# Kernel optimization log

Hardware: AMD Instinct MI355X
Metric: run time of the kernel (lower is better)

## Reference

```python
import jax, jax.numpy as jnp
import numpy as np

B, S, D, H = 2, 2048, 1024, 16
HD = D // H  # 64


def setup_inputs() -> dict:
    key = jax.random.key(0)
    ks = jax.random.split(key, 9)
    sd = 1.0 / np.sqrt(D)  # torch Linear default init scale (uniform, but normal ok for ref)
    return {
        "x": jax.random.normal(ks[0], (B, S, D), dtype=jnp.float32),
        # torch Linear weight is [out, in]; stack per head -> [H, HD, D]
        "Wq": jax.random.normal(ks[1], (H, HD, D), dtype=jnp.float32) * sd,
        "bq": jax.random.normal(ks[2], (H, HD), dtype=jnp.float32) * sd,
        "Wk": jax.random.normal(ks[3], (H, HD, D), dtype=jnp.float32) * sd,
        "bk": jax.random.normal(ks[4], (H, HD), dtype=jnp.float32) * sd,
        "Wv": jax.random.normal(ks[5], (H, HD, D), dtype=jnp.float32) * sd,
        "bv": jax.random.normal(ks[6], (H, HD), dtype=jnp.float32) * sd,
        "Wp": jax.random.normal(ks[7], (D, D), dtype=jnp.float32) * sd,
        "bp": jax.random.normal(ks[8], (D,), dtype=jnp.float32) * sd,
    }


def reference(x, Wq, bq, Wk, bk, Wv, bv, Wp, bp):
    # Per-head QKV projections, batched over heads: [B,S,D] x [H,HD,D] -> [B,H,S,HD]
    q = jnp.einsum("bsd,hed->bhse", x, Wq) + bq[None, :, None, :]
    k = jnp.einsum("bsd,hed->bhse", x, Wk) + bk[None, :, None, :]
    v = jnp.einsum("bsd,hed->bhse", x, Wv) + bv[None, :, None, :]
    scale = 1.0 / np.sqrt(HD)
    scores = jnp.einsum("bhse,bhte->bhst", q, k) * scale  # [B,H,S,S]
    attn = jax.nn.softmax(scores, axis=-1)
    out = jnp.einsum("bhst,bhte->bhse", attn, v)  # [B,H,S,HD]
    # concat heads along last dim (head-major order matches torch.cat over heads)
    out = out.transpose(0, 2, 1, 3).reshape(x.shape[0], x.shape[1], -1)  # [B,S,D]
    return out @ Wp.T + bp
```

## Files before the change

### kernel.cpp

```cpp
#include <hip/hip_runtime.h>
#include <hip/hip_bf16.h>
#include <stdint.h>

#define B_  2
#define S_  2048
#define D_  1024
#define H_  16
#define HD_ 64
#define M_  (B_*S_)
#define BH_ (B_*H_)

typedef __bf16 bf16;
typedef bf16  bf16x8 __attribute__((ext_vector_type(8)));
typedef bf16  bf16x4 __attribute__((ext_vector_type(4)));
typedef bf16  bf16x2 __attribute__((ext_vector_type(2)));
typedef float f32x4  __attribute__((ext_vector_type(4)));

#define SCALE_LOG2E 0.18033688011112042f
#define MFIX_LOG2E  23.083120654223415f

__device__ __forceinline__ f32x4 mfma16(bf16x8 a, bf16x8 b, f32x4 c) {
    return __builtin_amdgcn_mfma_f32_16x16x32_bf16(a, b, c, 0, 0, 0);
}
__device__ __forceinline__ float fexp2(float x) {
    return __builtin_amdgcn_exp2f(x);
}

__device__ __forceinline__ void gload_lds16(const bf16* g, bf16* l) {
    auto* gp = reinterpret_cast<__attribute__((address_space(1))) uint32_t*>(
        reinterpret_cast<uintptr_t>(const_cast<bf16*>(g)));
    auto* lp = reinterpret_cast<__attribute__((address_space(3))) uint32_t*>(
        reinterpret_cast<uintptr_t>(l));
    __builtin_amdgcn_global_load_lds(gp, lp, 16, 0, 0);
}

__global__ __launch_bounds__(256) void k_convert(
        const float* __restrict__ x,
        const float* __restrict__ wq, const float* __restrict__ wk,
        const float* __restrict__ wv, const float* __restrict__ wp,
        bf16* __restrict__ xb,
        bf16* __restrict__ wqb, bf16* __restrict__ wkb,
        bf16* __restrict__ wvb, bf16* __restrict__ wpb) {
    const int y = blockIdx.y;
    const float* src = (y == 0) ? x : (y == 1) ? wq : (y == 2) ? wk
                     : (y == 3) ? wv : wp;
    bf16* dst        = (y == 0) ? xb : (y == 1) ? wqb : (y == 2) ? wkb
                     : (y == 3) ? wvb : wpb;
    const int reps = (y == 0) ? 4 : 1;
    const int idx = blockIdx.x * 256 + threadIdx.x;
    for (int rep = 0; rep < reps; ++rep) {
        const size_t e = (size_t)rep * (1u << 20) + (size_t)idx * 4;
        const float4 f = *(const float4*)(src + e);
        bf16x4 o;
        o[0] = (bf16)f.x; o[1] = (bf16)f.y; o[2] = (bf16)f.z; o[3] = (bf16)f.w;
        *(bf16x4*)(dst + e) = o;
    }
}

__global__ __launch_bounds__(256) void k_gemm_qkv(
        const bf16* __restrict__ x,
        const bf16* __restrict__ Wq, const bf16* __restrict__ Wk, const bf16* __restrict__ Wv,
        const float* __restrict__ bq, const float* __restrict__ bk, const float* __restrict__ bv,
        bf16* __restrict__ q, bf16* __restrict__ k, bf16* __restrict__ vt) {
    const int z = blockIdx.z;
    const bf16* A   = x;
    const bf16* Bt  = (z == 0) ? Wq : (z == 1) ? Wk : Wv;
    const float* bias = (z == 0) ? bq : (z == 1) ? bk : bv;
    bf16* C         = (z == 0) ? q  : (z == 1) ? k  : vt;

    __shared__ bf16 As[2][128*32];
    __shared__ bf16 Bs[2][128*32];
    const int K = D_;
    const int NIT = K / 32;
    const int tid = threadIdx.x;
    const int w  = tid >> 6, L = tid & 63;
    const int lr = L & 15,  lq = L >> 4;
    const int tileM = blockIdx.y * 128, tileN = blockIdx.x * 128;
    const int wm = (w >> 1) * 64, wn = (w & 1) * 64;

    const f32x4 fzero = {0.f, 0.f, 0.f, 0.f};
    f32x4 acc[4][4];
#pragma unroll
    for (int i = 0; i < 4; ++i)
#pragma unroll
        for (int j = 0; j < 4; ++j) acc[i][j] = fzero;

    const int srow   = L >> 2;
    const int schunk = (L & 3) ^ (srow & 3);
    const bf16* ag = A  + (size_t)(tileM + w*32 + srow) * K + schunk*8;
    const bf16* bg = Bt + (size_t)(tileN + w*32 + srow) * K + schunk*8;
    const int sbase = (w*32)*32;
    const int sw = lr & 3;

    gload_lds16(ag,          &As[0][sbase]);
    gload_lds16(ag + 16*K,   &As[0][sbase + 16*32]);
    gload_lds16(bg,          &Bs[0][sbase]);
    gload_lds16(bg + 16*K,   &Bs[0][sbase + 16*32]);
    __syncthreads();

    for (int it = 0; it < NIT; ++it) {
        const int cur = it & 1, nxt = cur ^ 1;
        if (it + 1 < NIT) {
            const int kt = (it + 1) * 32;
            gload_lds16(ag + kt,          &As[nxt][sbase]);
            gload_lds16(ag + kt + 16*K,   &As[nxt][sbase + 16*32]);
            gload_lds16(bg + kt,          &Bs[nxt][sbase]);
            gload_lds16(bg + kt + 16*K,   &Bs[nxt][sbase + 16*32]);
        }

        bf16x8 af[4], bfr[4];
#pragma unroll
        for (int i = 0; i < 4; ++i)
            af[i]  = *(const bf16x8*)&As[cur][(wm + i*16 + lr)*32 + ((lq ^ sw) * 8)];
#pragma unroll
        for (int j = 0; j < 4; ++j)
            bfr[j] = *(const bf16x8*)&Bs[cur][(wn + j*16 + lr)*32 + ((lq ^ sw) * 8)];
#pragma unroll
        for (int i = 0; i < 4; ++i)
#pragma unroll
            for (int j = 0; j < 4; ++j)
                acc[i][j] = mfma16(af[i], bfr[j], acc[i][j]);

        if (it + 1 < NIT) __syncthreads();
    }

#pragma unroll
    for (int i = 0; i < 4; ++i) {
#pragma unroll
        for (int j = 0; j < 4; ++j) {
            const int m0 = tileM + wm + i*16 + lq*4;
            const int n  = tileN + wn + j*16 + lr;
            const int h = n >> 6, e = n & 63;
            if (z != 2) {
#pragma unroll
                for (int r = 0; r < 4; ++r) {
                    const int m = m0 + r;
                    const int b = m >> 11, s = m & (S_ - 1);
                    C[((size_t)((b*H_ + h)*S_ + s) << 6) + e] =
                        (bf16)(acc[i][j][r] + bias[n]);
                }
            } else {
                const int b = m0 >> 11, s0 = m0 & (S_ - 1);
                const float bn = bias[n];
                bf16x4 t4;
#pragma unroll
                for (int r = 0; r < 4; ++r) t4[r] = (bf16)(acc[i][j][r] + bn);
                *(bf16x4*)&C[(((size_t)(b*H_ + h)*HD_ + e) << 11) + s0] = t4;
            }
        }
    }
}

__global__ __launch_bounds__(256, 4) void k_gemm_proj(
        const bf16* __restrict__ A, const bf16* __restrict__ Bt,
        const float* __restrict__ bias, float* __restrict__ C) {
    __shared__ bf16 As[2][64*32];
    __shared__ bf16 Bs[2][64*32];
    const int K = D_;
    const int NIT = K / 32;
    const int tid = threadIdx.x;
    const int w  = tid >> 6, L = tid & 63;
    const int lr = L & 15,  lq = L >> 4;
    const int tileM = blockIdx.y * 64, tileN = blockIdx.x * 64;
    const int wm = (w >> 1) * 32, wn = (w & 1) * 32;

    const f32x4 fzero = {0.f, 0.f, 0.f, 0.f};
    f32x4 acc[2][2];
#pragma unroll
    for (int i = 0; i < 2; ++i)
#pragma unroll
        for (int j = 0; j < 2; ++j) acc[i][j] = fzero;

    const int srow   = L >> 2;
    const int schunk = (L & 3) ^ (srow & 3);
    const bf16* ag = A  + (size_t)(tileM + w*16 + srow) * K + schunk*8;
    const bf16* bg = Bt + (size_t)(tileN + w*16 + srow) * K + schunk*8;
    const int sbase = (w*16)*32;
    const int sw = lr & 3;

    gload_lds16(ag, &As[0][sbase]);
    gload_lds16(bg, &Bs[0][sbase]);
    __syncthreads();

    for (int it = 0; it < NIT; ++it) {
        const int cur = it & 1, nxt = cur ^ 1;
        if (it + 1 < NIT) {
            const int kt = (it + 1) * 32;
            gload_lds16(ag + kt, &As[nxt][sbase]);
            gload_lds16(bg + kt, &Bs[nxt][sbase]);
        }

        bf16x8 af[2], bfr[2];
#pragma unroll
        for (int i = 0; i < 2; ++i)
            af[i]  = *(const bf16x8*)&As[cur][(wm + i*16 + lr)*32 + ((lq ^ sw) * 8)];
#pragma unroll
        for (int j = 0; j < 2; ++j)
            bfr[j] = *(const bf16x8*)&Bs[cur][(wn + j*16 + lr)*32 + ((lq ^ sw) * 8)];
#pragma unroll
        for (int i = 0; i < 2; ++i)
#pragma unroll
            for (int j = 0; j < 2; ++j)
                acc[i][j] = mfma16(af[i], bfr[j], acc[i][j]);

        if (it + 1 < NIT) __syncthreads();
    }

#pragma unroll
    for (int i = 0; i < 2; ++i) {
#pragma unroll
        for (int j = 0; j < 2; ++j) {
#pragma unroll
            for (int r = 0; r < 4; ++r) {
                const int m = tileM + wm + i*16 + lq*4 + r;
                const int n = tileN + wn + j*16 + lr;
                C[(size_t)m * D_ + n] = acc[i][j][r] + bias[n];
            }
        }
    }
}

__global__ __launch_bounds__(256, 2) void k_attn(const bf16* __restrict__ Q,
                                                 const bf16* __restrict__ Kg,
                                                 const bf16* __restrict__ Vt,
                                                 bf16* __restrict__ O) {
    __shared__ bf16 Ks[2][64*64];
    __shared__ bf16 Vs[2][64*64];
    __shared__ bf16 Ps[4*32*64];
    const int tid = threadIdx.x;
    const int w  = tid >> 6, L = tid & 63;
    const int lr = L & 15,  lq = L >> 4;
    const int bh = blockIdx.y;
    const int q0 = blockIdx.x * 128 + w * 32;
    const size_t base = (size_t)bh * S_ * HD_;
    const bf16* qp = Q  + base;
    const bf16* kp = Kg + base;
    const bf16* vp = Vt + base;

    bf16x8 qf[2][2];
#pragma unroll
    for (int h2 = 0; h2 < 2; ++h2) {
        qf[h2][0] = *(const bf16x8*)&qp[(q0 + h2*16 + lr)*HD_ + lq*8];
        qf[h2][1] = *(const bf16x8*)&qp[(q0 + h2*16 + lr)*HD_ + 32 + lq*8];
    }

    const int rbase = (w & 1) * 32;
    const int srow  = L >> 3;
    const int gchunk = (L & 7) ^ srow;

    const int c0 = ((lq ^ (lr & 7))) * 8;
    const int c1 = ((lq ^ (lr & 7)) ^ 4) * 8;
    const int pxor = lr & 7;

    const f32x4 fzero = {0.f, 0.f, 0.f, 0.f};
    float l_lane[2] = {0.f, 0.f};
    f32x4 o_acc[2][4];
#pragma unroll
    for (int h2 = 0; h2 < 2; ++h2)
#pragma unroll
        for (int eb = 0; eb < 4; ++eb) o_acc[h2][eb] = fzero;

    bf16* myP = &Ps[w * 32 * 64];

    if (w < 2) {
#pragma unroll
        for (int i = 0; i < 4; ++i)
            gload_lds16(kp + (size_t)(rbase + i*8 + srow)*HD_ + gchunk*8,
                        &Ks[0][(rbase + i*8)*HD_]);
    } else {
#pragma unroll
        for (int i = 0; i < 4; ++i)
            gload_lds16(vp + (size_t)(rbase + i*8 + srow)*S_ + gchunk*8,
                        &Vs[0][(rbase + i*8)*HD_]);
    }
    __syncthreads();

    for (int it = 0; it < S_/64; ++it) {
        const int cur = it & 1, nxt = cur ^ 1;
        if (it + 1 < S_/64) {
            const int t1 = (it + 1) * 64;
            if (w < 2) {
#pragma unroll
                for (int i = 0; i < 4; ++i)
                    gload_lds16(kp + (size_t)(t1 + rbase + i*8 + srow)*HD_ + gchunk*8,
                                &Ks[nxt][(rbase + i*8)*HD_]);
            } else {
#pragma unroll
                for (int i = 0; i < 4; ++i)
                    gload_lds16(vp + (size_t)(rbase + i*8 + srow)*S_ + t1 + gchunk*8,
                                &Vs[nxt][(rbase + i*8)*HD_]);
            }
        }

#pragma unroll
        for (int j = 0; j < 4; ++j) {
            const bf16x8 kf0 = *(const bf16x8*)&Ks[cur][(j*16 + lr)*HD_ + c0];
            const bf16x8 kf1 = *(const bf16x8*)&Ks[cur][(j*16 + lr)*HD_ + c1];
            const int key0 = j*16 + lq*4;
            const int poff = ((key0 >> 3) ^ pxor)*8 + (key0 & 7);
#pragma unroll
            for (int h2 = 0; h2 < 2; ++h2) {
                f32x4 z = fzero;
                z = mfma16(kf0, qf[h2][0], z);
                z = mfma16(kf1, qf[h2][1], z);
                bf16x4 t4;
                float ls = 0.f;
#pragma unroll
                for (int r = 0; r < 4; ++r) {
                    const float pv = fexp2(
                        __builtin_fmaf(z[r], SCALE_LOG2E, -MFIX_LOG2E));
                    ls += pv;
                    t4[r] = (bf16)pv;
                }
                l_lane[h2] += ls;
                *(bf16x4*)&myP[(h2*16 + lr)*64 + poff] = t4;
            }
        }

        bf16x8 pb[2][2];
#pragma unroll
        for (int h2 = 0; h2 < 2; ++h2) {
            pb[h2][0] = *(const bf16x8*)&myP[(h2*16 + lr)*64 + ((lq     ^ pxor))*8];
            pb[h2][1] = *(const bf16x8*)&myP[(h2*16 + lr)*64 + (((4+lq) ^ pxor))*8];
        }
#pragma unroll
        for (int eb = 0; eb < 4; ++eb) {
            const bf16x8 vb0 = *(const bf16x8*)&Vs[cur][(eb*16 + lr)*HD_ + c0];
            const bf16x8 vb1 = *(const bf16x8*)&Vs[cur][(eb*16 + lr)*HD_ + c1];
#pragma unroll
            for (int h2 = 0; h2 < 2; ++h2) {
                o_acc[h2][eb] = mfma16(vb0, pb[h2][0], o_acc[h2][eb]);
                o_acc[h2][eb] = mfma16(vb1, pb[h2][1], o_acc[h2][eb]);
            }
        }

        if (it + 1 < S_/64) __syncthreads();
    }

    const int b = bh >> 4, h = bh & 15;
#pragma unroll
    for (int h2 = 0; h2 < 2; ++h2) {
        float l = l_lane[h2];
        l += __shfl_xor(l, 16);
        l += __shfl_xor(l, 32);
        const float inv = 1.f / l;
        const size_t obase = ((size_t)(b*S_ + q0 + h2*16 + lr))*D_ + h*64;
#pragma unroll
        for (int eb = 0; eb < 4; ++eb)
#pragma unroll
            for (int b2 = 0; b2 < 2; ++b2) {
                bf16x2 t2 = { (bf16)(o_acc[h2][eb][2*b2]   * inv),
                              (bf16)(o_acc[h2][eb][2*b2+1] * inv) };
                *(bf16x2*)&O[obase + eb*16 + lq*4 + 2*b2] = t2;
            }
    }
}

extern "C" void kernel_launch(void* const* d_in, const int* in_sizes, int n_in,
                              void* d_out, int out_size, void* d_ws, size_t ws_size,
                              hipStream_t stream) {
    const float* x  = (const float*)d_in[0];
    const float* Wq = (const float*)d_in[1];
    const float* bq = (const float*)d_in[2];
    const float* Wk = (const float*)d_in[3];
    const float* bk = (const float*)d_in[4];
    const float* Wv = (const float*)d_in[5];
    const float* bv = (const float*)d_in[6];
    const float* Wp = (const float*)d_in[7];
    const float* bp = (const float*)d_in[8];
    float* out = (float*)d_out;

    const size_t NE = (size_t)B_ * H_ * S_ * HD_;
    const size_t NW = (size_t)D_ * D_;
    bf16* xb  = (bf16*)d_ws;
    bf16* wqb = xb + NE;
    bf16* wkb = wqb + NW;
    bf16* wvb = wkb + NW;
    bf16* wpb = wvb + NW;
    bf16* q_ws  = wpb + NW;
    bf16* k_ws  = q_ws + NE;
    bf16* vt_ws = k_ws + NE;
    bf16* a_ws  = xb;

    k_convert<<<dim3(1024, 5), 256, 0, stream>>>(x, Wq, Wk, Wv, Wp,
                                                 xb, wqb, wkb, wvb, wpb);
    k_gemm_qkv<<<dim3(D_/128, M_/128, 3), 256, 0, stream>>>(
        xb, wqb, wkb, wvb, bq, bk, bv, q_ws, k_ws, vt_ws);
    k_attn<<<dim3(S_/128, BH_), 256, 0, stream>>>(q_ws, k_ws, vt_ws, a_ws);
    k_gemm_proj<<<dim3(D_/64, M_/64), 256, 0, stream>>>(a_ws, wpb, bp, out);
}
```

Baseline: 195.2 us.

## Load K/V fragments directly from global in attention and widen QKV GEMM k-tile

In the attention kernel the shared-memory double buffers for K and V are removed. Each wave now loads its K and V fragments straight from global memory into registers, prefetching the next K tile, and the per-block barriers go away. The row-sum is computed with an extra MFMA against a ones vector, which replaces the scalar accumulation and shuffles. The QKV GEMM switches from a double-buffered 32-wide k-tile to a single-buffered 64-wide tile with two barriers per step. Each wave now fetches K/V redundantly from global/L2 with no cross-wave sharing, and the GEMM loses its load/compute overlap.

Measured after the change: 267.0 us. 36.8% more time.

```diff
diff --git a/kernel.cpp b/kernel.cpp
--- a/kernel.cpp
+++ b/kernel.cpp
@@ -68,10 +68,9 @@
     const float* bias = (z == 0) ? bq : (z == 1) ? bk : bv;
     bf16* C         = (z == 0) ? q  : (z == 1) ? k  : vt;
 
-    __shared__ bf16 As[2][128*32];
-    __shared__ bf16 Bs[2][128*32];
+    __shared__ bf16 As[128*64];
+    __shared__ bf16 Bs[128*64];
     const int K = D_;
-    const int NIT = K / 32;
     const int tid = threadIdx.x;
     const int w  = tid >> 6, L = tid & 63;
     const int lr = L & 15,  lq = L >> 4;
@@ -85,43 +84,38 @@
 #pragma unroll
         for (int j = 0; j < 4; ++j) acc[i][j] = fzero;
 
-    const int srow   = L >> 2;
-    const int schunk = (L & 3) ^ (srow & 3);
-    const bf16* ag = A  + (size_t)(tileM + w*32 + srow) * K + schunk*8;
-    const bf16* bg = Bt + (size_t)(tileN + w*32 + srow) * K + schunk*8;
-    const int sbase = (w*32)*32;
-    const int sw = lr & 3;
-
-    gload_lds16(ag,          &As[0][sbase]);
-    gload_lds16(ag + 16*K,   &As[0][sbase + 16*32]);
-    gload_lds16(bg,          &Bs[0][sbase]);
-    gload_lds16(bg + 16*K,   &Bs[0][sbase + 16*32]);
-    __syncthreads();
-
-    for (int it = 0; it < NIT; ++it) {
-        const int cur = it & 1, nxt = cur ^ 1;
-        if (it + 1 < NIT) {
-            const int kt = (it + 1) * 32;
-            gload_lds16(ag + kt,          &As[nxt][sbase]);
-            gload_lds16(ag + kt + 16*K,   &As[nxt][sbase + 16*32]);
-            gload_lds16(bg + kt,          &Bs[nxt][sbase]);
-            gload_lds16(bg + kt + 16*K,   &Bs[nxt][sbase + 16*32]);
-        }
-
-        bf16x8 af[4], bfr[4];
-#pragma unroll
-        for (int i = 0; i < 4; ++i)
-            af[i]  = *(const bf16x8*)&As[cur][(wm + i*16 + lr)*32 + ((lq ^ sw) * 8)];
-#pragma unroll
-        for (int j = 0; j < 4; ++j)
-            bfr[j] = *(const bf16x8*)&Bs[cur][(wn + j*16 + lr)*32 + ((lq ^ sw) * 8)];
-#pragma unroll
-        for (int i = 0; i < 4; ++i)
+    const int srow8 = L >> 3;
+    const int gch8  = (L & 7) ^ srow8;
+    const bf16* ag = A  + (size_t)(tileM + w*32 + srow8) * K + gch8*8;
+    const bf16* bg = Bt + (size_t)(tileN + w*32 + srow8) * K + gch8*8;
+    const int sb = (w*32)*64;
+    const int fx = lr & 7;
+
+    for (int kt = 0; kt < K; kt += 64) {
+        __syncthreads();
+#pragma unroll
+        for (int i = 0; i < 4; ++i) {
+            gload_lds16(ag + kt + (size_t)(i*8)*K, &As[sb + (i*8)*64]);
+            gload_lds16(bg + kt + (size_t)(i*8)*K, &Bs[sb + (i*8)*64]);
+        }
+        __syncthreads();
+
+#pragma unroll
+        for (int s = 0; s < 2; ++s) {
+            const int co = (((s*4 + lq) ^ fx)) * 8;
+            bf16x8 af[4], bfr[4];
+#pragma unroll
+            for (int i = 0; i < 4; ++i)
+                af[i]  = *(const bf16x8*)&As[(wm + i*16 + lr)*64 + co];
 #pragma unroll
             for (int j = 0; j < 4; ++j)
-                acc[i][j] = mfma16(af[i], bfr[j], acc[i][j]);
-
-        if (it + 1 < NIT) __syncthreads();
+                bfr[j] = *(const bf16x8*)&Bs[(wn + j*16 + lr)*64 + co];
+#pragma unroll
+            for (int i = 0; i < 4; ++i)
+#pragma unroll
+                for (int j = 0; j < 4; ++j)
+                    acc[i][j] = mfma16(af[i], bfr[j], acc[i][j]);
+        }
     }
 
 #pragma unroll
@@ -220,12 +214,10 @@
     }
 }
 
-__global__ __launch_bounds__(256, 2) void k_attn(const bf16* __restrict__ Q,
-                                                 const bf16* __restrict__ Kg,
-                                                 const bf16* __restrict__ Vt,
-                                                 bf16* __restrict__ O) {
-    __shared__ bf16 Ks[2][64*64];
-    __shared__ bf16 Vs[2][64*64];
+__global__ __launch_bounds__(256) void k_attn(const bf16* __restrict__ Q,
+                                              const bf16* __restrict__ Kg,
+                                              const bf16* __restrict__ Vt,
+                                              bf16* __restrict__ O) {
     __shared__ bf16 Ps[4*32*64];
     const int tid = threadIdx.x;
     const int w  = tid >> 6, L = tid & 63;
@@ -244,76 +236,65 @@
         qf[h2][1] = *(const bf16x8*)&qp[(q0 + h2*16 + lr)*HD_ + 32 + lq*8];
     }
 
-    const int rbase = (w & 1) * 32;
-    const int srow  = L >> 3;
-    const int gchunk = (L & 7) ^ srow;
-
-    const int c0 = ((lq ^ (lr & 7))) * 8;
-    const int c1 = ((lq ^ (lr & 7)) ^ 4) * 8;
+    bf16x8 kone;
+#pragma unroll
+    for (int i = 0; i < 8; ++i) kone[i] = (bf16)1.0f;
+
     const int pxor = lr & 7;
 
     const f32x4 fzero = {0.f, 0.f, 0.f, 0.f};
-    float l_lane[2] = {0.f, 0.f};
     f32x4 o_acc[2][4];
-#pragma unroll
-    for (int h2 = 0; h2 < 2; ++h2)
+    f32x4 o_l[2];
+#pragma unroll
+    for (int h2 = 0; h2 < 2; ++h2) {
+        o_l[h2] = fzero;
 #pragma unroll
         for (int eb = 0; eb < 4; ++eb) o_acc[h2][eb] = fzero;
+    }
 
     bf16* myP = &Ps[w * 32 * 64];
 
-    if (w < 2) {
-#pragma unroll
-        for (int i = 0; i < 4; ++i)
-            gload_lds16(kp + (size_t)(rbase + i*8 + srow)*HD_ + gchunk*8,
-                        &Ks[0][(rbase + i*8)*HD_]);
-    } else {
-#pragma unroll
-        for (int i = 0; i < 4; ++i)
-            gload_lds16(vp + (size_t)(rbase + i*8 + srow)*S_ + gchunk*8,
-                        &Vs[0][(rbase + i*8)*HD_]);
-    }
-    __syncthreads();
-
-    for (int it = 0; it < S_/64; ++it) {
-        const int cur = it & 1, nxt = cur ^ 1;
-        if (it + 1 < S_/64) {
-            const int t1 = (it + 1) * 64;
-            if (w < 2) {
-#pragma unroll
-                for (int i = 0; i < 4; ++i)
-                    gload_lds16(kp + (size_t)(t1 + rbase + i*8 + srow)*HD_ + gchunk*8,
-                                &Ks[nxt][(rbase + i*8)*HD_]);
-            } else {
-#pragma unroll
-                for (int i = 0; i < 4; ++i)
-                    gload_lds16(vp + (size_t)(rbase + i*8 + srow)*S_ + t1 + gchunk*8,
-                                &Vs[nxt][(rbase + i*8)*HD_]);
-            }
+    bf16x8 kf[4][2];
+#pragma unroll
+    for (int j = 0; j < 4; ++j) {
+        const bf16* kr = &kp[(size_t)(j*16 + lr) * HD_];
+        kf[j][0] = *(const bf16x8*)&kr[lq*8];
+        kf[j][1] = *(const bf16x8*)&kr[32 + lq*8];
+    }
+
+    for (int t0 = 0; t0 < S_; t0 += 64) {
+        bf16x8 vf[4][2];
+#pragma unroll
+        for (int eb = 0; eb < 4; ++eb) {
+            const bf16* vr = &vp[(size_t)(eb*16 + lr) * S_ + t0];
+            vf[eb][0] = *(const bf16x8*)&vr[lq*8];
+            vf[eb][1] = *(const bf16x8*)&vr[32 + lq*8];
         }
 
 #pragma unroll
         for (int j = 0; j < 4; ++j) {
-            const bf16x8 kf0 = *(const bf16x8*)&Ks[cur][(j*16 + lr)*HD_ + c0];
-            const bf16x8 kf1 = *(const bf16x8*)&Ks[cur][(j*16 + lr)*HD_ + c1];
             const int key0 = j*16 + lq*4;
             const int poff = ((key0 >> 3) ^ pxor)*8 + (key0 & 7);
 #pragma unroll
             for (int h2 = 0; h2 < 2; ++h2) {
                 f32x4 z = fzero;
-                z = mfma16(kf0, qf[h2][0], z);
-                z = mfma16(kf1, qf[h2][1], z);
+                z = mfma16(kf[j][0], qf[h2][0], z);
+                z = mfma16(kf[j][1], qf[h2][1], z);
                 bf16x4 t4;
-                float ls = 0.f;
-#pragma unroll
-                for (int r = 0; r < 4; ++r) {
-                    const float pv = fexp2(
+#pragma unroll
+                for (int r = 0; r < 4; ++r)
+                    t4[r] = (bf16)fexp2(
                         __builtin_fmaf(z[r], SCALE_LOG2E, -MFIX_LOG2E));
-                    ls += pv;
-                    t4[r] = (bf16)pv;
-                }
-                l_lane[h2] += ls;
                 *(bf16x4*)&myP[(h2*16 + lr)*64 + poff] = t4;
+            }
+        }
+
+        if (t0 + 64 < S_) {
+#pragma unroll
+            for (int j = 0; j < 4; ++j) {
+                const bf16* kr = &kp[(size_t)(t0 + 64 + j*16 + lr) * HD_];
+                kf[j][0] = *(const bf16x8*)&kr[lq*8];
+                kf[j][1] = *(const bf16x8*)&kr[32 + lq*8];
             }
         }
 
@@ -323,27 +304,25 @@
             pb[h2][0] = *(const bf16x8*)&myP[(h2*16 + lr)*64 + ((lq     ^ pxor))*8];
             pb[h2][1] = *(const bf16x8*)&myP[(h2*16 + lr)*64 + (((4+lq) ^ pxor))*8];
         }
-#pragma unroll
-        for (int eb = 0; eb < 4; ++eb) {
-            const bf16x8 vb0 = *(const bf16x8*)&Vs[cur][(eb*16 + lr)*HD_ + c0];
-            const bf16x8 vb1 = *(const bf16x8*)&Vs[cur][(eb*16 + lr)*HD_ + c1];
+
+#pragma unroll
+        for (int eb = 0; eb < 4; ++eb)
 #pragma unroll
             for (int h2 = 0; h2 < 2; ++h2) {
-                o_acc[h2][eb] = mfma16(vb0, pb[h2][0], o_acc[h2][eb]);
-                o_acc[h2][eb] = mfma16(vb1, pb[h2][1], o_acc[h2][eb]);
-            }
-        }
-
-        if (it + 1 < S_/64) __syncthreads();
+                o_acc[h2][eb] = mfma16(vf[eb][0], pb[h2][0], o_acc[h2][eb]);
+                o_acc[h2][eb] = mfma16(vf[eb][1], pb[h2][1], o_acc[h2][eb]);
+            }
+#pragma unroll
+        for (int h2 = 0; h2 < 2; ++h2) {
+            o_l[h2] = mfma16(kone, pb[h2][0], o_l[h2]);
+            o_l[h2] = mfma16(kone, pb[h2][1], o_l[h2]);
+        }
     }
 
     const int b = bh >> 4, h = bh & 15;
 #pragma unroll
     for (int h2 = 0; h2 < 2; ++h2) {
-        float l = l_lane[h2];
-        l += __shfl_xor(l, 16);
-        l += __shfl_xor(l, 32);
-        const float inv = 1.f / l;
+        const float inv = 1.f / o_l[h2][0];
         const size_t obase = ((size_t)(b*S_ + q0 + h2*16 + lr))*D_ + h*64;
 #pragma unroll
         for (int eb = 0; eb < 4; ++eb)
```
